# Kernel tuning notes

Measured on AMD Instinct MI355X. Metric: run time of the kernel, lower is better.

The kernel has to match this reference:

```python
import jax, jax.numpy as jnp
import numpy as np

N_NODES = 100000
N_EDGES = 1600000
IN_FEATS = 128
HIDDEN = 150
NUM_OUT = 128


def setup_inputs() -> dict:
    key = jax.random.key(0)
    ks = jax.random.split(key, 9)
    x = jax.random.normal(ks[0], (N_NODES, IN_FEATS), dtype=jnp.float32)
    src = jax.random.randint(ks[1], (N_EDGES,), 0, N_NODES, dtype=jnp.int32)
    dst = jax.random.randint(ks[2], (N_EDGES,), 0, N_NODES, dtype=jnp.int32)
    def lin(k, fan_in, fan_out):
        bound = 1.0 / np.sqrt(fan_in)
        return jax.random.uniform(k, (fan_in, fan_out), jnp.float32, -bound, bound)
    W_self1 = lin(ks[3], IN_FEATS, HIDDEN)
    W_neigh1 = lin(ks[4], IN_FEATS, HIDDEN)
    b1 = jnp.zeros((HIDDEN,), jnp.float32)
    W_self2 = lin(ks[5], HIDDEN, NUM_OUT)
    W_neigh2 = lin(ks[6], HIDDEN, NUM_OUT)
    b2 = jnp.zeros((NUM_OUT,), jnp.float32)
    return {"x": x, "src": src, "dst": dst,
            "W_self1": W_self1, "W_neigh1": W_neigh1, "b1": b1,
            "W_self2": W_self2, "W_neigh2": W_neigh2, "b2": b2}


def _mean_agg(h, src, dst, deg_inv):
    # segment-mean of source features onto destination nodes; isolated nodes -> 0
    summed = jax.ops.segment_sum(h[src], dst, num_segments=N_NODES)
    return summed * deg_inv[:, None]


def _sage_conv(h, src, dst, deg_inv, W_self, W_neigh, b):
    h_neigh = _mean_agg(h, src, dst, deg_inv)
    return h @ W_self + h_neigh @ W_neigh + b


def reference(x, src, dst, W_self1, W_neigh1, b1, W_self2, W_neigh2, b2):
    deg = jax.ops.segment_sum(jnp.ones((src.shape[0],), x.dtype), dst,
                              num_segments=N_NODES)
    deg_inv = jnp.where(deg > 0, 1.0 / jnp.maximum(deg, 1.0), 0.0)
    h = _sage_conv(x, src, dst, deg_inv, W_self1, W_neigh1, b1)
    h = jax.nn.relu(h)
    h = _sage_conv(h, src, dst, deg_inv, W_self2, W_neigh2, b2)
    return h
```

## Files before the change

### kernel.cpp

```cpp
#include <hip/hip_runtime.h>

#define NN 100000
#define NE 1600000
#define INF 128
#define HID 150
#define NOUT 128

#define NBK 196
#define WGS 400
#define EPW 4000
#define CNTL (NBK * WGS)
#define CAP2 10240

typedef __attribute__((ext_vector_type(8))) short bf16x8;
typedef __attribute__((ext_vector_type(8))) unsigned short u16x8;
typedef __attribute__((ext_vector_type(4))) float f32x4;

__device__ inline unsigned short f2bf(float f) {
    unsigned int u = __float_as_uint(f);
    u += 0x7fffu + ((u >> 16) & 1u);
    return (unsigned short)(u >> 16);
}
__device__ inline float bflo(unsigned int t) { return __uint_as_float(t << 16); }
__device__ inline float bfhi(unsigned int t) { return __uint_as_float(t & 0xffff0000u); }


__global__ __launch_bounds__(256) void sort1(const int* __restrict__ src,
                                             const int* __restrict__ dst,
                                             unsigned int* __restrict__ chunkw,
                                             int* __restrict__ cntm) {
    __shared__ int hist[NBK];
    __shared__ int off[NBK];
    __shared__ int s[256];
    __shared__ unsigned int buf[EPW];
    int w = blockIdx.x, tid = threadIdx.x;
    int e0 = w * EPW;
    for (int i = tid; i < NBK; i += 256) hist[i] = 0;
    __syncthreads();
    for (int i = tid; i < EPW; i += 256) atomicAdd(&hist[dst[e0 + i] >> 9], 1);
    __syncthreads();
    int v = (tid < NBK) ? hist[tid] : 0;
    s[tid] = v;
    __syncthreads();
    for (int o = 1; o < 256; o <<= 1) {
        int t = (tid >= o) ? s[tid - o] : 0;
        __syncthreads();
        s[tid] += t;
        __syncthreads();
    }
    if (tid < NBK) {
        off[tid] = s[tid] - v;
        cntm[tid * WGS + w] = v;
    }
    __syncthreads();
    for (int i = tid; i < EPW; i += 256) {
        int d = dst[e0 + i];
        int b = d >> 9;
        int p = atomicAdd(&off[b], 1);
        buf[p] = (unsigned int)src[e0 + i] | ((unsigned int)(d & 511) << 17);
    }
    __syncthreads();
    for (int i = tid; i < EPW; i += 256) chunkw[e0 + i] = buf[i];
}

__global__ void scanA(const int* __restrict__ in, int* __restrict__ excl,
                      int* __restrict__ blk_sums, int L) {
    __shared__ int s[256];
    int i = blockIdx.x * 256 + threadIdx.x;
    int d = (i < L) ? in[i] : 0;
    s[threadIdx.x] = d;
    __syncthreads();
    for (int o = 1; o < 256; o <<= 1) {
        int t = (threadIdx.x >= o) ? s[threadIdx.x - o] : 0;
        __syncthreads();
        s[threadIdx.x] += t;
        __syncthreads();
    }
    int incl = s[threadIdx.x];
    if (i < L) excl[i] = incl - d;
    if (threadIdx.x == 255) blk_sums[blockIdx.x] = incl;
}

__global__ void scanB(int* __restrict__ blk_sums, int nb) {
    __shared__ int s[512];
    int t = threadIdx.x;
    int v = (t < nb) ? blk_sums[t] : 0;
    s[t] = v;
    __syncthreads();
    for (int o = 1; o < 512; o <<= 1) {
        int u = (t >= o) ? s[t - o] : 0;
        __syncthreads();
        s[t] += u;
        __syncthreads();
    }
    if (t < nb) blk_sums[t] = s[t] - v;
}

__global__ void scanC(int* __restrict__ excl, const int* __restrict__ blk_sums, int L) {
    int i = blockIdx.x * 256 + threadIdx.x;
    if (i < L) excl[i] += blk_sums[blockIdx.x];
}

__global__ __launch_bounds__(256) void sort3(const unsigned int* __restrict__ chunkw,
                                             const int* __restrict__ cntm,
                                             const int* __restrict__ offm,
                                             unsigned int* __restrict__ bmaj) {
    __shared__ int excl[NBK + 1];
    __shared__ int dbase[NBK];
    __shared__ int s[256];
    int w = blockIdx.x, tid = threadIdx.x;
    int v = (tid < NBK) ? cntm[tid * WGS + w] : 0;
    if (tid < NBK) dbase[tid] = offm[tid * WGS + w];
    s[tid] = v;
    __syncthreads();
    for (int o = 1; o < 256; o <<= 1) {
        int t = (tid >= o) ? s[tid - o] : 0;
        __syncthreads();
        s[tid] += t;
        __syncthreads();
    }
    if (tid < NBK) excl[tid] = s[tid] - v;
    if (tid == 0) excl[NBK] = EPW;
    __syncthreads();
    int e0 = w * EPW;
    for (int i = tid; i < EPW; i += 256) {
        int lo = 0, hi = NBK;
        while (hi - lo > 1) {
            int mid = (lo + hi) >> 1;
            if (excl[mid] <= i) lo = mid; else hi = mid;
        }
        bmaj[dbase[lo] + (i - excl[lo])] = chunkw[e0 + i];
    }
}

__global__ __launch_bounds__(256) void buildcsr(const unsigned int* __restrict__ bmaj,
                                                const int* __restrict__ offm,
                                                int* __restrict__ csr_ptr,
                                                float* __restrict__ deg_inv,
                                                int* __restrict__ csr_src) {
    __shared__ int cnt[512];
    __shared__ int excl[512];
    __shared__ int off[512];
    __shared__ int s[256];
    __shared__ int span[CAP2];
    int b = blockIdx.x, tid = threadIdx.x;
    int base = offm[b * WGS];
    int nxt = (b == NBK - 1) ? NE : offm[(b + 1) * WGS];
    int n = nxt - base;
    if (n > CAP2) n = CAP2;
    for (int i = tid; i < 512; i += 256) cnt[i] = 0;
    __syncthreads();
    for (int i = tid; i < n; i += 256) atomicAdd(&cnt[bmaj[base + i] >> 17], 1);
    __syncthreads();
    int a0 = cnt[2 * tid], a1 = cnt[2 * tid + 1];
    int ps = a0 + a1;
    s[tid] = ps;
    __syncthreads();
    for (int o = 1; o < 256; o <<= 1) {
        int t = (tid >= o) ? s[tid - o] : 0;
        __syncthreads();
        s[tid] += t;
        __syncthreads();
    }
    int ex = s[tid] - ps;
    excl[2 * tid] = ex;
    excl[2 * tid + 1] = ex + a0;
    off[2 * tid] = ex;
    off[2 * tid + 1] = ex + a0;
    __syncthreads();
    for (int l = tid; l < 512; l += 256) {
        int g = b * 512 + l;
        if (g < NN) {
            csr_ptr[g] = base + excl[l];
            int d = cnt[l];
            deg_inv[g] = d > 0 ? 1.0f / (float)d : 0.0f;
        }
    }
    if (b == NBK - 1 && tid == 0) csr_ptr[NN] = NE;
    for (int i = tid; i < n; i += 256) {
        unsigned int wd = bmaj[base + i];
        int l = wd >> 17;
        int p = atomicAdd(&off[l], 1);
        span[p] = (int)(wd & 0x1FFFFu);
    }
    __syncthreads();
    for (int i = tid; i < n; i += 256) csr_src[base + i] = span[i];
}


__global__ void cast_bf16(const float* __restrict__ in, unsigned short* __restrict__ outb,
                          int n8) {
    int i = blockIdx.x * 256 + threadIdx.x;
    if (i >= n8) return;
    const float4* p = (const float4*)in;
    float4 v0 = p[(size_t)i * 2];
    float4 v1 = p[(size_t)i * 2 + 1];
    u16x8 o = {f2bf(v0.x), f2bf(v0.y), f2bf(v0.z), f2bf(v0.w),
               f2bf(v1.x), f2bf(v1.y), f2bf(v1.z), f2bf(v1.w)};
    ((u16x8*)outb)[i] = o;
}

__global__ void pack_weights(const float* __restrict__ Ws1, const float* __restrict__ Wn1,
                             const float* __restrict__ b1,
                             const float* __restrict__ Ws2, const float* __restrict__ Wn2,
                             unsigned short* __restrict__ W1t, unsigned short* __restrict__ W2t,
                             float* __restrict__ b1p) {
    int id = blockIdx.x * 256 + threadIdx.x;
    if (id < 160 * 256) {
        int n = id >> 8, k = id & 255;
        float v = 0.f;
        if (n < HID) v = (k < 128) ? Ws1[k * HID + n] : Wn1[(k - 128) * HID + n];
        W1t[id] = f2bf(v);
    } else if (id < 160 * 256 + 256 * 160) {
        int id2 = id - 160 * 256;
        int n = id2 / 160, k = id2 - n * 160;
        float v = 0.f;
        if (k < HID) v = (n < 128) ? Ws2[k * 128 + n] : Wn2[k * 128 + (n - 128)];
        W2t[id2] = f2bf(v);
    } else if (id < 160 * 256 + 256 * 160 + 160) {
        int n = id - (160 * 256 + 256 * 160);
        b1p[n] = (n < HID) ? b1[n] : 0.f;
    }
}


#define AGG_ACC(t)                    \
    acc0 += bflo(t.x); acc1 += bfhi(t.x); \
    acc2 += bflo(t.y); acc3 += bfhi(t.y); \
    acc4 += bflo(t.z); acc5 += bfhi(t.z); \
    acc6 += bflo(t.w); acc7 += bfhi(t.w);

__global__ __launch_bounds__(256) void agg_mean_q(
    const unsigned short* __restrict__ featb, const int* __restrict__ csr_ptr,
    const float* __restrict__ deg_inv, const int* __restrict__ csr_src,
    unsigned short* __restrict__ outb) {
    int wid = threadIdx.x >> 6;
    int lane = threadIdx.x & 63;
    int v = blockIdx.x * 4 + wid;
    int start = csr_ptr[v], end = csr_ptr[v + 1];
    int rg = lane >> 4, ch = lane & 15;
    const uint4* f4 = (const uint4*)featb;
    float acc0 = 0.f, acc1 = 0.f, acc2 = 0.f, acc3 = 0.f;
    float acc4 = 0.f, acc5 = 0.f, acc6 = 0.f, acc7 = 0.f;
    int e = start;
    for (; e + 8 <= end; e += 8) {
        int s0 = csr_src[e + rg];
        int s1 = csr_src[e + 4 + rg];
        uint4 t0 = f4[(size_t)s0 * 16 + ch];
        uint4 t1 = f4[(size_t)s1 * 16 + ch];
        AGG_ACC(t0);
        AGG_ACC(t1);
    }
    if (e + 4 <= end) {
        int s0 = csr_src[e + rg];
        uint4 t0 = f4[(size_t)s0 * 16 + ch];
        AGG_ACC(t0);
        e += 4;
    }
    int rem = end - e;
    if (rem > 0) {
        int s0 = csr_src[(rg < rem) ? (e + rg) : e];
        uint4 t = f4[(size_t)s0 * 16 + ch];
        float wt = (rg < rem) ? 1.f : 0.f;
        acc0 += wt * bflo(t.x); acc1 += wt * bfhi(t.x);
        acc2 += wt * bflo(t.y); acc3 += wt * bfhi(t.y);
        acc4 += wt * bflo(t.z); acc5 += wt * bfhi(t.z);
        acc6 += wt * bflo(t.w); acc7 += wt * bfhi(t.w);
    }
    acc0 += __shfl_xor(acc0, 32); acc1 += __shfl_xor(acc1, 32);
    acc2 += __shfl_xor(acc2, 32); acc3 += __shfl_xor(acc3, 32);
    acc4 += __shfl_xor(acc4, 32); acc5 += __shfl_xor(acc5, 32);
    acc6 += __shfl_xor(acc6, 32); acc7 += __shfl_xor(acc7, 32);
    acc0 += __shfl_xor(acc0, 16); acc1 += __shfl_xor(acc1, 16);
    acc2 += __shfl_xor(acc2, 16); acc3 += __shfl_xor(acc3, 16);
    acc4 += __shfl_xor(acc4, 16); acc5 += __shfl_xor(acc5, 16);
    acc6 += __shfl_xor(acc6, 16); acc7 += __shfl_xor(acc7, 16);
    if (lane < 16) {
        float di = deg_inv[v];
        u16x8 o = {f2bf(acc0 * di), f2bf(acc1 * di), f2bf(acc2 * di), f2bf(acc3 * di),
                   f2bf(acc4 * di), f2bf(acc5 * di), f2bf(acc6 * di), f2bf(acc7 * di)};
        ((u16x8*)outb)[(size_t)v * 16 + ch] = o;
    }
}

__global__ __launch_bounds__(256) void agg_add_q(
    const unsigned short* __restrict__ zb, const int* __restrict__ csr_ptr,
    const float* __restrict__ deg_inv, const int* __restrict__ csr_src,
    float* __restrict__ out) {
    int wid = threadIdx.x >> 6;
    int lane = threadIdx.x & 63;
    int v = blockIdx.x * 4 + wid;
    int start = csr_ptr[v], end = csr_ptr[v + 1];
    int rg = lane >> 4, ch = lane & 15;
    const uint4* f4 = (const uint4*)zb;
    float acc0 = 0.f, acc1 = 0.f, acc2 = 0.f, acc3 = 0.f;
    float acc4 = 0.f, acc5 = 0.f, acc6 = 0.f, acc7 = 0.f;
    int e = start;
    for (; e + 8 <= end; e += 8) {
        int s0 = csr_src[e + rg];
        int s1 = csr_src[e + 4 + rg];
        uint4 t0 = f4[(size_t)s0 * 16 + ch];
        uint4 t1 = f4[(size_t)s1 * 16 + ch];
        AGG_ACC(t0);
        AGG_ACC(t1);
    }
    if (e + 4 <= end) {
        int s0 = csr_src[e + rg];
        uint4 t0 = f4[(size_t)s0 * 16 + ch];
        AGG_ACC(t0);
        e += 4;
    }
    int rem = end - e;
    if (rem > 0) {
        int s0 = csr_src[(rg < rem) ? (e + rg) : e];
        uint4 t = f4[(size_t)s0 * 16 + ch];
        float wt = (rg < rem) ? 1.f : 0.f;
        acc0 += wt * bflo(t.x); acc1 += wt * bfhi(t.x);
        acc2 += wt * bflo(t.y); acc3 += wt * bfhi(t.y);
        acc4 += wt * bflo(t.z); acc5 += wt * bfhi(t.z);
        acc6 += wt * bflo(t.w); acc7 += wt * bfhi(t.w);
    }
    acc0 += __shfl_xor(acc0, 32); acc1 += __shfl_xor(acc1, 32);
    acc2 += __shfl_xor(acc2, 32); acc3 += __shfl_xor(acc3, 32);
    acc4 += __shfl_xor(acc4, 32); acc5 += __shfl_xor(acc5, 32);
    acc6 += __shfl_xor(acc6, 32); acc7 += __shfl_xor(acc7, 32);
    acc0 += __shfl_xor(acc0, 16); acc1 += __shfl_xor(acc1, 16);
    acc2 += __shfl_xor(acc2, 16); acc3 += __shfl_xor(acc3, 16);
    acc4 += __shfl_xor(acc4, 16); acc5 += __shfl_xor(acc5, 16);
    acc6 += __shfl_xor(acc6, 16); acc7 += __shfl_xor(acc7, 16);
    if (lane < 16) {
        float di = deg_inv[v];
        float4* o4 = (float4*)out;
        size_t base = (size_t)v * 32 + ch * 2;
        float4 c0 = o4[base];
        float4 c1 = o4[base + 1];
        c0.x += acc0 * di; c0.y += acc1 * di; c0.z += acc2 * di; c0.w += acc3 * di;
        c1.x += acc4 * di; c1.y += acc5 * di; c1.z += acc6 * di; c1.w += acc7 * di;
        o4[base] = c0;
        o4[base + 1] = c1;
    }
}


__global__ __launch_bounds__(256) void gemm1_mfma(
    const unsigned short* __restrict__ xb, const unsigned short* __restrict__ aggb,
    const unsigned short* __restrict__ W1t, const float* __restrict__ b1p,
    unsigned short* __restrict__ h1b) {
    __shared__ __align__(16) unsigned short A_lds[128][40];
    __shared__ __align__(16) unsigned short B_lds[160][40];
    int tid = threadIdx.x;
    int m0 = blockIdx.x * 128;
    int w = tid >> 6, lane = tid & 63;
    int lrow = lane & 15, quad = lane >> 4;
    int wr = (w & 1) * 64;
    int wc = (w >> 1) * 80;
    f32x4 acc[4][5];
    #pragma unroll
    for (int r = 0; r < 4; r++)
        #pragma unroll
        for (int c = 0; c < 5; c++) acc[r][c] = (f32x4){0.f, 0.f, 0.f, 0.f};

    for (int k0 = 0; k0 < 256; k0 += 32) {
        __syncthreads();
        #pragma unroll
        for (int i = 0; i < 2; i++) {
            int idx = tid + i * 256;
            int row = idx >> 2, ch = idx & 3;
            int gm = m0 + row, gk = k0 + ch * 8;
            u16x8 val = {0, 0, 0, 0, 0, 0, 0, 0};
            if (gm < NN) {
                const unsigned short* sp = (gk < 128)
                    ? (xb + (size_t)gm * 128 + gk)
                    : (aggb + (size_t)gm * 128 + (gk - 128));
                val = *(const u16x8*)sp;
            }
            *(u16x8*)&A_lds[row][ch * 8] = val;
        }
        #pragma unroll
        for (int i = 0; i < 3; i++) {
            int idx = tid + i * 256;
            if (idx < 640) {
                int n = idx >> 2, ch = idx & 3;
                u16x8 val = *(const u16x8*)(W1t + (size_t)n * 256 + k0 + ch * 8);
                *(u16x8*)&B_lds[n][ch * 8] = val;
            }
        }
        __syncthreads();
        bf16x8 a[4], b[5];
        #pragma unroll
        for (int r = 0; r < 4; r++)
            a[r] = *(const bf16x8*)&A_lds[wr + r * 16 + lrow][quad * 8];
        #pragma unroll
        for (int c = 0; c < 5; c++)
            b[c] = *(const bf16x8*)&B_lds[wc + c * 16 + lrow][quad * 8];
        #pragma unroll
        for (int r = 0; r < 4; r++)
            #pragma unroll
            for (int c = 0; c < 5; c++)
                acc[r][c] = __builtin_amdgcn_mfma_f32_16x16x32_bf16(a[r], b[c], acc[r][c], 0, 0, 0);
    }
    #pragma unroll
    for (int r = 0; r < 4; r++) {
        #pragma unroll
        for (int rr = 0; rr < 4; rr++) {
            int gm = m0 + wr + r * 16 + quad * 4 + rr;
            if (gm < NN) {
                #pragma unroll
                for (int c = 0; c < 5; c++) {
                    int gn = wc + c * 16 + lrow;
                    float val = acc[r][c][rr] + b1p[gn];
                    val = val > 0.f ? val : 0.f;
                    h1b[(size_t)gm * 160 + gn] = f2bf(val);
                }
            }
        }
    }
}

__global__ __launch_bounds__(256) void gemm2_mfma(
    const unsigned short* __restrict__ h1b, const unsigned short* __restrict__ W2t,
    const float* __restrict__ b2, float* __restrict__ out,
    unsigned short* __restrict__ zb) {
    __shared__ __align__(16) unsigned short A_lds[128][40];
    __shared__ __align__(16) unsigned short B_lds[128][40];
    int tid = threadIdx.x;
    int m0 = blockIdx.x * 128;
    int n0 = blockIdx.y * 128;
    int w = tid >> 6, lane = tid & 63;
    int lrow = lane & 15, quad = lane >> 4;
    int wr = (w & 1) * 64;
    int wc = (w >> 1) * 64;
    f32x4 acc[4][4];
    #pragma unroll
    for (int r = 0; r < 4; r++)
        #pragma unroll
        for (int c = 0; c < 4; c++) acc[r][c] = (f32x4){0.f, 0.f, 0.f, 0.f};

    for (int k0 = 0; k0 < 160; k0 += 32) {
        __syncthreads();
        #pragma unroll
        for (int i = 0; i < 2; i++) {
            int idx = tid + i * 256;
            int row = idx >> 2, ch = idx & 3;
            int gm = m0 + row;
            u16x8 val = {0, 0, 0, 0, 0, 0, 0, 0};
            if (gm < NN) val = *(const u16x8*)(h1b + (size_t)gm * 160 + k0 + ch * 8);
            *(u16x8*)&A_lds[row][ch * 8] = val;
        }
        #pragma unroll
        for (int i = 0; i < 2; i++) {
            int idx = tid + i * 256;
            int n = idx >> 2, ch = idx & 3;
            u16x8 val = *(const u16x8*)(W2t + (size_t)(n0 + n) * 160 + k0 + ch * 8);
            *(u16x8*)&B_lds[n][ch * 8] = val;
        }
        __syncthreads();
        bf16x8 a[4], b[4];
        #pragma unroll
        for (int r = 0; r < 4; r++)
            a[r] = *(const bf16x8*)&A_lds[wr + r * 16 + lrow][quad * 8];
        #pragma unroll
        for (int c = 0; c < 4; c++)
            b[c] = *(const bf16x8*)&B_lds[wc + c * 16 + lrow][quad * 8];
        #pragma unroll
        for (int r = 0; r < 4; r++)
            #pragma unroll
            for (int c = 0; c < 4; c++)
                acc[r][c] = __builtin_amdgcn_mfma_f32_16x16x32_bf16(a[r], b[c], acc[r][c], 0, 0, 0);
    }
    #pragma unroll
    for (int r = 0; r < 4; r++) {
        #pragma unroll
        for (int rr = 0; rr < 4; rr++) {
            int gm = m0 + wr + r * 16 + quad * 4 + rr;
            if (gm < NN) {
                #pragma unroll
                for (int c = 0; c < 4; c++) {
                    int gn = wc + c * 16 + lrow;
                    float val = acc[r][c][rr];
                    if (n0 == 0) {
                        out[(size_t)gm * 128 + gn] = val + b2[gn];
                    } else {
                        zb[(size_t)gm * 128 + gn] = f2bf(val);
                    }
                }
            }
        }
    }
}


extern "C" void kernel_launch(void* const* d_in, const int* in_sizes, int n_in,
                              void* d_out, int out_size, void* d_ws, size_t ws_size,
                              hipStream_t stream) {
    const float* x   = (const float*)d_in[0];
    const int* src   = (const int*)d_in[1];
    const int* dst   = (const int*)d_in[2];
    const float* Ws1 = (const float*)d_in[3];
    const float* Wn1 = (const float*)d_in[4];
    const float* b1  = (const float*)d_in[5];
    const float* Ws2 = (const float*)d_in[6];
    const float* Wn2 = (const float*)d_in[7];
    const float* b2  = (const float*)d_in[8];
    float* out = (float*)d_out;

    char* p = (char*)d_ws;
    auto carve = [&](size_t bytes) {
        void* r = (void*)p;
        p += (bytes + 255) & ~(size_t)255;
        return r;
    };
    int*   csr_ptr  = (int*)carve((size_t)(NN + 1) * 4);
    float* deg_inv  = (float*)carve((size_t)NN * 4);
    int*   csr_src  = (int*)carve((size_t)NE * 4);
    int*   cntm     = (int*)carve((size_t)CNTL * 4);
    int*   offm     = (int*)carve((size_t)CNTL * 4);
    int*   blk2     = (int*)carve(512 * 4);
    unsigned short* xb   = (unsigned short*)carve((size_t)NN * 128 * 2);
    unsigned short* aggb = (unsigned short*)carve((size_t)NN * 128 * 2);
    unsigned short* zb   = (unsigned short*)carve((size_t)NN * 128 * 2);
    unsigned short* W1t  = (unsigned short*)carve(160 * 256 * 2);
    unsigned short* W2t  = (unsigned short*)carve(256 * 160 * 2);
    float* b1p           = (float*)carve(160 * 4);
    unsigned short* h1b  = (unsigned short*)carve((size_t)NN * 160 * 2);
    unsigned int* chunkw = (unsigned int*)h1b;
    unsigned int* bmaj   = (unsigned int*)((char*)h1b + (size_t)NE * 4);

    sort1<<<WGS, 256, 0, stream>>>(src, dst, chunkw, cntm);
    const int SB = (CNTL + 255) / 256;
    scanA<<<SB, 256, 0, stream>>>(cntm, offm, blk2, CNTL);
    scanB<<<1, 512, 0, stream>>>(blk2, SB);
    scanC<<<SB, 256, 0, stream>>>(offm, blk2, CNTL);
    sort3<<<WGS, 256, 0, stream>>>(chunkw, cntm, offm, bmaj);
    buildcsr<<<NBK, 256, 0, stream>>>(bmaj, offm, csr_ptr, deg_inv, csr_src);

    cast_bf16<<<(NN * 128 / 8 + 255) / 256, 256, 0, stream>>>(x, xb, NN * 128 / 8);
    pack_weights<<<(160 * 256 + 256 * 160 + 160 + 255) / 256, 256, 0, stream>>>(
        Ws1, Wn1, b1, Ws2, Wn2, W1t, W2t, b1p);

    agg_mean_q<<<NN / 4, 256, 0, stream>>>(xb, csr_ptr, deg_inv, csr_src, aggb);
    gemm1_mfma<<<dim3((NN + 127) / 128, 1), 256, 0, stream>>>(xb, aggb, W1t, b1p, h1b);

    gemm2_mfma<<<dim3((NN + 127) / 128, 2), 256, 0, stream>>>(h1b, W2t, b2, out, zb);
    agg_add_q<<<NN / 4, 256, 0, stream>>>(zb, csr_ptr, deg_inv, csr_src, out);

    (void)in_sizes; (void)n_in; (void)out_size; (void)ws_size;
}
```

Before: 387.5 us.

## Merge three-pass scan into one kernel, unroll aggregation, add nontemporal loads

Replaces the three-kernel block scan over the 78400 bucket counts with a single 1024-thread workgroup that serially sums per-thread chunks, scans in LDS, and writes exclusive offsets. This removes two kernel launches and their dependencies. The aggregation loops now issue four neighbour gathers per iteration instead of two for more memory-level parallelism, at some register cost. Nontemporal loads and stores are used for the x cast and the output read-modify-write. The single-block scan reads strided chunks uncoalesced on one CU, which could offset the saved launches.

```diff
diff --git a/kernel.cpp b/kernel.cpp
--- a/kernel.cpp
+++ b/kernel.cpp
@@ -63,42 +63,33 @@
     for (int i = tid; i < EPW; i += 256) chunkw[e0 + i] = buf[i];
 }
 
-__global__ void scanA(const int* __restrict__ in, int* __restrict__ excl,
-                      int* __restrict__ blk_sums, int L) {
-    __shared__ int s[256];
-    int i = blockIdx.x * 256 + threadIdx.x;
-    int d = (i < L) ? in[i] : 0;
-    s[threadIdx.x] = d;
-    __syncthreads();
-    for (int o = 1; o < 256; o <<= 1) {
-        int t = (threadIdx.x >= o) ? s[threadIdx.x - o] : 0;
-        __syncthreads();
-        s[threadIdx.x] += t;
-        __syncthreads();
-    }
-    int incl = s[threadIdx.x];
-    if (i < L) excl[i] = incl - d;
-    if (threadIdx.x == 255) blk_sums[blockIdx.x] = incl;
-}
-
-__global__ void scanB(int* __restrict__ blk_sums, int nb) {
-    __shared__ int s[512];
+__global__ __launch_bounds__(1024) void scan_all(const int* __restrict__ in,
+                                                 int* __restrict__ excl) {
+    __shared__ int s[1024];
+    const int C = (CNTL + 1023) / 1024;
     int t = threadIdx.x;
-    int v = (t < nb) ? blk_sums[t] : 0;
-    s[t] = v;
-    __syncthreads();
-    for (int o = 1; o < 512; o <<= 1) {
-        int u = (t >= o) ? s[t - o] : 0;
-        __syncthreads();
-        s[t] += u;
-        __syncthreads();
-    }
-    if (t < nb) blk_sums[t] = s[t] - v;
-}
-
-__global__ void scanC(int* __restrict__ excl, const int* __restrict__ blk_sums, int L) {
-    int i = blockIdx.x * 256 + threadIdx.x;
-    if (i < L) excl[i] += blk_sums[blockIdx.x];
+    int base = t * C;
+    int sum = 0;
+    for (int i = 0; i < C; i++) {
+        int idx = base + i;
+        if (idx < CNTL) sum += in[idx];
+    }
+    s[t] = sum;
+    __syncthreads();
+    for (int o = 1; o < 1024; o <<= 1) {
+        int v = (t >= o) ? s[t - o] : 0;
+        __syncthreads();
+        s[t] += v;
+        __syncthreads();
+    }
+    int run = s[t] - sum;
+    for (int i = 0; i < C; i++) {
+        int idx = base + i;
+        if (idx < CNTL) {
+            excl[idx] = run;
+            run += in[idx];
+        }
+    }
 }
 
 __global__ __launch_bounds__(256) void sort3(const unsigned int* __restrict__ chunkw,
@@ -192,11 +183,11 @@
                           int n8) {
     int i = blockIdx.x * 256 + threadIdx.x;
     if (i >= n8) return;
-    const float4* p = (const float4*)in;
-    float4 v0 = p[(size_t)i * 2];
-    float4 v1 = p[(size_t)i * 2 + 1];
-    u16x8 o = {f2bf(v0.x), f2bf(v0.y), f2bf(v0.z), f2bf(v0.w),
-               f2bf(v1.x), f2bf(v1.y), f2bf(v1.z), f2bf(v1.w)};
+    const f32x4* p = (const f32x4*)in;
+    f32x4 v0 = __builtin_nontemporal_load(&p[(size_t)i * 2]);
+    f32x4 v1 = __builtin_nontemporal_load(&p[(size_t)i * 2 + 1]);
+    u16x8 o = {f2bf(v0[0]), f2bf(v0[1]), f2bf(v0[2]), f2bf(v0[3]),
+               f2bf(v1[0]), f2bf(v1[1]), f2bf(v1[2]), f2bf(v1[3])};
     ((u16x8*)outb)[i] = o;
 }
 
@@ -230,6 +221,56 @@
     acc4 += bflo(t.z); acc5 += bfhi(t.z); \
     acc6 += bflo(t.w); acc7 += bfhi(t.w);
 
+#define AGG_BODY(FTBL)                                                 \
+    int e = start;                                                     \
+    for (; e + 16 <= end; e += 16) {                                   \
+        int s0 = csr_src[e + rg];                                      \
+        int s1 = csr_src[e + 4 + rg];                                  \
+        int s2 = csr_src[e + 8 + rg];                                  \
+        int s3 = csr_src[e + 12 + rg];                                 \
+        uint4 t0 = FTBL[(size_t)s0 * 16 + ch];                         \
+        uint4 t1 = FTBL[(size_t)s1 * 16 + ch];                         \
+        uint4 t2 = FTBL[(size_t)s2 * 16 + ch];                         \
+        uint4 t3 = FTBL[(size_t)s3 * 16 + ch];                         \
+        AGG_ACC(t0);                                                   \
+        AGG_ACC(t1);                                                   \
+        AGG_ACC(t2);                                                   \
+        AGG_ACC(t3);                                                   \
+    }                                                                  \
+    if (e + 8 <= end) {                                                \
+        int s0 = csr_src[e + rg];                                      \
+        int s1 = csr_src[e + 4 + rg];                                  \
+        uint4 t0 = FTBL[(size_t)s0 * 16 + ch];                         \
+        uint4 t1 = FTBL[(size_t)s1 * 16 + ch];                         \
+        AGG_ACC(t0);                                                   \
+        AGG_ACC(t1);                                                   \
+        e += 8;                                                        \
+    }                                                                  \
+    if (e + 4 <= end) {                                                \
+        int s0 = csr_src[e + rg];                                      \
+        uint4 t0 = FTBL[(size_t)s0 * 16 + ch];                         \
+        AGG_ACC(t0);                                                   \
+        e += 4;                                                        \
+    }                                                                  \
+    int rem = end - e;                                                 \
+    if (rem > 0) {                                                     \
+        int s0 = csr_src[(rg < rem) ? (e + rg) : e];                   \
+        uint4 t = FTBL[(size_t)s0 * 16 + ch];                          \
+        float wt = (rg < rem) ? 1.f : 0.f;                             \
+        acc0 += wt * bflo(t.x); acc1 += wt * bfhi(t.x);                \
+        acc2 += wt * bflo(t.y); acc3 += wt * bfhi(t.y);                \
+        acc4 += wt * bflo(t.z); acc5 += wt * bfhi(t.z);                \
+        acc6 += wt * bflo(t.w); acc7 += wt * bfhi(t.w);                \
+    }                                                                  \
+    acc0 += __shfl_xor(acc0, 32); acc1 += __shfl_xor(acc1, 32);        \
+    acc2 += __shfl_xor(acc2, 32); acc3 += __shfl_xor(acc3, 32);        \
+    acc4 += __shfl_xor(acc4, 32); acc5 += __shfl_xor(acc5, 32);        \
+    acc6 += __shfl_xor(acc6, 32); acc7 += __shfl_xor(acc7, 32);        \
+    acc0 += __shfl_xor(acc0, 16); acc1 += __shfl_xor(acc1, 16);        \
+    acc2 += __shfl_xor(acc2, 16); acc3 += __shfl_xor(acc3, 16);        \
+    acc4 += __shfl_xor(acc4, 16); acc5 += __shfl_xor(acc5, 16);        \
+    acc6 += __shfl_xor(acc6, 16); acc7 += __shfl_xor(acc7, 16);
+
 __global__ __launch_bounds__(256) void agg_mean_q(
     const unsigned short* __restrict__ featb, const int* __restrict__ csr_ptr,
     const float* __restrict__ deg_inv, const int* __restrict__ csr_src,
@@ -242,39 +283,7 @@
     const uint4* f4 = (const uint4*)featb;
     float acc0 = 0.f, acc1 = 0.f, acc2 = 0.f, acc3 = 0.f;
     float acc4 = 0.f, acc5 = 0.f, acc6 = 0.f, acc7 = 0.f;
-    int e = start;
-    for (; e + 8 <= end; e += 8) {
-        int s0 = csr_src[e + rg];
-        int s1 = csr_src[e + 4 + rg];
-        uint4 t0 = f4[(size_t)s0 * 16 + ch];
-        uint4 t1 = f4[(size_t)s1 * 16 + ch];
-        AGG_ACC(t0);
-        AGG_ACC(t1);
-    }
-    if (e + 4 <= end) {
-        int s0 = csr_src[e + rg];
-        uint4 t0 = f4[(size_t)s0 * 16 + ch];
-        AGG_ACC(t0);
-        e += 4;
-    }
-    int rem = end - e;
-    if (rem > 0) {
-        int s0 = csr_src[(rg < rem) ? (e + rg) : e];
-        uint4 t = f4[(size_t)s0 * 16 + ch];
-        float wt = (rg < rem) ? 1.f : 0.f;
-        acc0 += wt * bflo(t.x); acc1 += wt * bfhi(t.x);
-        acc2 += wt * bflo(t.y); acc3 += wt * bfhi(t.y);
-        acc4 += wt * bflo(t.z); acc5 += wt * bfhi(t.z);
-        acc6 += wt * bflo(t.w); acc7 += wt * bfhi(t.w);
-    }
-    acc0 += __shfl_xor(acc0, 32); acc1 += __shfl_xor(acc1, 32);
-    acc2 += __shfl_xor(acc2, 32); acc3 += __shfl_xor(acc3, 32);
-    acc4 += __shfl_xor(acc4, 32); acc5 += __shfl_xor(acc5, 32);
-    acc6 += __shfl_xor(acc6, 32); acc7 += __shfl_xor(acc7, 32);
-    acc0 += __shfl_xor(acc0, 16); acc1 += __shfl_xor(acc1, 16);
-    acc2 += __shfl_xor(acc2, 16); acc3 += __shfl_xor(acc3, 16);
-    acc4 += __shfl_xor(acc4, 16); acc5 += __shfl_xor(acc5, 16);
-    acc6 += __shfl_xor(acc6, 16); acc7 += __shfl_xor(acc7, 16);
+    AGG_BODY(f4);
     if (lane < 16) {
         float di = deg_inv[v];
         u16x8 o = {f2bf(acc0 * di), f2bf(acc1 * di), f2bf(acc2 * di), f2bf(acc3 * di),
@@ -295,49 +304,17 @@
     const uint4* f4 = (const uint4*)zb;
     float acc0 = 0.f, acc1 = 0.f, acc2 = 0.f, acc3 = 0.f;
     float acc4 = 0.f, acc5 = 0.f, acc6 = 0.f, acc7 = 0.f;
-    int e = start;
-    for (; e + 8 <= end; e += 8) {
-        int s0 = csr_src[e + rg];
-        int s1 = csr_src[e + 4 + rg];
-        uint4 t0 = f4[(size_t)s0 * 16 + ch];
-        uint4 t1 = f4[(size_t)s1 * 16 + ch];
-        AGG_ACC(t0);
-        AGG_ACC(t1);
-    }
-    if (e + 4 <= end) {
-        int s0 = csr_src[e + rg];
-        uint4 t0 = f4[(size_t)s0 * 16 + ch];
-        AGG_ACC(t0);
-        e += 4;
-    }
-    int rem = end - e;
-    if (rem > 0) {
-        int s0 = csr_src[(rg < rem) ? (e + rg) : e];
-        uint4 t = f4[(size_t)s0 * 16 + ch];
-        float wt = (rg < rem) ? 1.f : 0.f;
-        acc0 += wt * bflo(t.x); acc1 += wt * bfhi(t.x);
-        acc2 += wt * bflo(t.y); acc3 += wt * bfhi(t.y);
-        acc4 += wt * bflo(t.z); acc5 += wt * bfhi(t.z);
-        acc6 += wt * bflo(t.w); acc7 += wt * bfhi(t.w);
-    }
-    acc0 += __shfl_xor(acc0, 32); acc1 += __shfl_xor(acc1, 32);
-    acc2 += __shfl_xor(acc2, 32); acc3 += __shfl_xor(acc3, 32);
-    acc4 += __shfl_xor(acc4, 32); acc5 += __shfl_xor(acc5, 32);
-    acc6 += __shfl_xor(acc6, 32); acc7 += __shfl_xor(acc7, 32);
-    acc0 += __shfl_xor(acc0, 16); acc1 += __shfl_xor(acc1, 16);
-    acc2 += __shfl_xor(acc2, 16); acc3 += __shfl_xor(acc3, 16);
-    acc4 += __shfl_xor(acc4, 16); acc5 += __shfl_xor(acc5, 16);
-    acc6 += __shfl_xor(acc6, 16); acc7 += __shfl_xor(acc7, 16);
+    AGG_BODY(f4);
     if (lane < 16) {
         float di = deg_inv[v];
-        float4* o4 = (float4*)out;
+        f32x4* o4 = (f32x4*)out;
         size_t base = (size_t)v * 32 + ch * 2;
-        float4 c0 = o4[base];
-        float4 c1 = o4[base + 1];
-        c0.x += acc0 * di; c0.y += acc1 * di; c0.z += acc2 * di; c0.w += acc3 * di;
-        c1.x += acc4 * di; c1.y += acc5 * di; c1.z += acc6 * di; c1.w += acc7 * di;
-        o4[base] = c0;
-        o4[base + 1] = c1;
+        f32x4 c0 = __builtin_nontemporal_load(&o4[base]);
+        f32x4 c1 = __builtin_nontemporal_load(&o4[base + 1]);
+        c0[0] += acc0 * di; c0[1] += acc1 * di; c0[2] += acc2 * di; c0[3] += acc3 * di;
+        c1[0] += acc4 * di; c1[1] += acc5 * di; c1[2] += acc6 * di; c1[3] += acc7 * di;
+        __builtin_nontemporal_store(c0, &o4[base]);
+        __builtin_nontemporal_store(c1, &o4[base + 1]);
     }
 }
 
@@ -515,7 +492,6 @@
     int*   csr_src  = (int*)carve((size_t)NE * 4);
     int*   cntm     = (int*)carve((size_t)CNTL * 4);
     int*   offm     = (int*)carve((size_t)CNTL * 4);
-    int*   blk2     = (int*)carve(512 * 4);
     unsigned short* xb   = (unsigned short*)carve((size_t)NN * 128 * 2);
     unsigned short* aggb = (unsigned short*)carve((size_t)NN * 128 * 2);
     unsigned short* zb   = (unsigned short*)carve((size_t)NN * 128 * 2);
@@ -527,10 +503,7 @@
     unsigned int* bmaj   = (unsigned int*)((char*)h1b + (size_t)NE * 4);
 
     sort1<<<WGS, 256, 0, stream>>>(src, dst, chunkw, cntm);
-    const int SB = (CNTL + 255) / 256;
-    scanA<<<SB, 256, 0, stream>>>(cntm, offm, blk2, CNTL);
-    scanB<<<1, 512, 0, stream>>>(blk2, SB);
-    scanC<<<SB, 256, 0, stream>>>(offm, blk2, CNTL);
+    scan_all<<<1, 1024, 0, stream>>>(cntm, offm);
     sort3<<<WGS, 256, 0, stream>>>(chunkw, cntm, offm, bmaj);
     buildcsr<<<NBK, 256, 0, stream>>>(bmaj, offm, csr_ptr, deg_inv, csr_src);
 
```

New measurement: 522.7 us. +34.9%, slower.
